# Optimization experiments

Measured on AMD Instinct MI355X. Metric: run time of the kernel, lower is better.

Reference implementation:

```python
import jax, jax.numpy as jnp
import numpy as np

B, IN, H, A, K = 8192, 2048, 256, 8192, 512

def setup_inputs() -> dict:
    key = jax.random.key(0)
    ks = jax.random.split(key, 8)
    s1, s2, s3 = 1.0/np.sqrt(IN), 1.0/np.sqrt(H), 1.0/np.sqrt(H)
    return {
        "x": jax.random.normal(ks[0], (B, IN), dtype=jnp.float32),
        "possible_moves": jax.random.randint(ks[1], (B, K), 0, A, dtype=jnp.int64),
        "W1": jax.random.uniform(ks[2], (IN, H), jnp.float32, -s1, s1),
        "b1": jax.random.uniform(ks[3], (H,), jnp.float32, -s1, s1),
        "W2": jax.random.uniform(ks[4], (H, H), jnp.float32, -s2, s2),
        "b2": jax.random.uniform(ks[5], (H,), jnp.float32, -s2, s2),
        "W3": jax.random.uniform(ks[6], (H, A), jnp.float32, -s3, s3),
        "b3": jax.random.uniform(ks[7], (A,), jnp.float32, -s3, s3),
    }

def reference(x, possible_moves, W1, b1, W2, b2, W3, b3):
    h = jax.nn.relu(x @ W1 + b1)
    h = jax.nn.relu(h @ W2 + b2)
    q = h @ W3 + b3                      # [B, A]
    # build per-sample legal-move mask via scatter (replaces torch python loop)
    rows = jnp.arange(q.shape[0])[:, None]
    mask = jnp.zeros(q.shape, q.dtype).at[rows, possible_moves].set(1.0)
    filtered = q * mask
    # faithful to torch: any exact-zero entry (illegal OR q==0) becomes -inf
    return jnp.where(filtered == 0, -jnp.inf, filtered)
```

## Files before the change

### kernel.cpp

```cpp
#include <hip/hip_runtime.h>
#include <math.h>
#include <stdint.h>

#define B_DIM   8192
#define IN_DIM  2048
#define H_DIM   256
#define A_DIM   8192
#define K_MOVES 512

#define NEG_SENTINEL (-3.0e38f)

typedef __attribute__((ext_vector_type(8))) short      short8;
typedef __attribute__((ext_vector_type(8))) unsigned short ushort8;
typedef __attribute__((ext_vector_type(4))) float      f32x4;

#define MFMA_16x16x32_BF16(a, b, c) \
    __builtin_amdgcn_mfma_f32_16x16x32_bf16((a), (b), (c), 0, 0, 0)

__device__ __forceinline__ unsigned short f2bf(float f) {
    union { float f; unsigned int u; } v; v.f = f;
    unsigned int r = v.u + 0x7fffu + ((v.u >> 16) & 1u);
    return (unsigned short)(r >> 16);
}

__global__ void zero_u64_kernel(unsigned long long* __restrict__ p, int n) {
    int i = blockIdx.x * 256 + threadIdx.x;
    if (i < n) p[i] = 0ULL;
}

__global__ void scatter_mask_kernel(const int* __restrict__ pm,
                                    unsigned long long* __restrict__ mask) {
    int i = blockIdx.x * 256 + threadIdx.x;
    int row = i / K_MOVES;
    int mv  = pm[i];
    if (mv < 0) mv = 0;
    if (mv >= A_DIM) mv = A_DIM - 1;
    atomicOr(&mask[(size_t)row * (A_DIM / 64) + (mv >> 6)],
             1ULL << (mv & 63));
}

__global__ void cvt_bf16_kernel(const float* __restrict__ in,
                                unsigned short* __restrict__ out, int n8) {
    int i = blockIdx.x * 256 + threadIdx.x;
    if (i >= n8) return;
    const float4* p = (const float4*)in + (size_t)i * 2;
    float4 a = p[0], b = p[1];
    ushort8 o;
    o[0] = f2bf(a.x); o[1] = f2bf(a.y); o[2] = f2bf(a.z); o[3] = f2bf(a.w);
    o[4] = f2bf(b.x); o[5] = f2bf(b.y); o[6] = f2bf(b.z); o[7] = f2bf(b.w);
    *(ushort8*)(out + (size_t)i * 8) = o;
}

__global__ __launch_bounds__(256)
void transpose_cvt_kernel(const float* __restrict__ in,
                          unsigned short* __restrict__ out, int R, int C) {
    __shared__ unsigned short tile[32][33];
    int x = blockIdx.x * 32 + threadIdx.x;
#pragma unroll
    for (int i = 0; i < 32; i += 8) {
        int y = blockIdx.y * 32 + threadIdx.y + i;
        tile[threadIdx.y + i][threadIdx.x] = f2bf(in[(size_t)y * C + x]);
    }
    __syncthreads();
    int ox = blockIdx.y * 32 + threadIdx.x;
#pragma unroll
    for (int i = 0; i < 32; i += 8) {
        int oy = blockIdx.x * 32 + threadIdx.y + i;
        out[(size_t)oy * R + ox] = tile[threadIdx.x][threadIdx.y + i];
    }
}

template <int RELU, int MASKED, typename OutT>
__global__ __launch_bounds__(256)
void gemm_bt_mfma(const unsigned short* __restrict__ A,
                  const unsigned short* __restrict__ Bt,
                  const float* __restrict__ bias,
                  OutT* __restrict__ C,
                  const unsigned long long* __restrict__ mask,
                  int M, int N, int K) {
    __shared__ __align__(16) unsigned short As[128 * 32];
    __shared__ __align__(16) unsigned short Bs[128 * 32];

    const int tid  = threadIdx.x;
    const int wave = tid >> 6;
    const int lane = tid & 63;
    const int quad = lane >> 4;
    const int tl   = lane & 15;
    const int wm   = wave >> 1;
    const int wn   = wave & 1;
    const int row0 = blockIdx.y * 128;
    const int col0 = blockIdx.x * 128;

    f32x4 acc[4][4];
#pragma unroll
    for (int i = 0; i < 4; ++i)
#pragma unroll
        for (int j = 0; j < 4; ++j) acc[i][j] = {0.f, 0.f, 0.f, 0.f};

    const int c0 = tid;
    const int c1 = 256 + tid;

    for (int k0 = 0; k0 < K; k0 += 32) {
        {
            const unsigned short* g0 = A + (size_t)(row0 + (c0 >> 2)) * K + k0 + (c0 & 3) * 8;
            const unsigned short* g1 = A + (size_t)(row0 + (c1 >> 2)) * K + k0 + (c1 & 3) * 8;
            __builtin_amdgcn_global_load_lds(
                (const __attribute__((address_space(1))) void*)g0,
                (__attribute__((address_space(3))) void*)&As[(wave * 64) * 8], 16, 0, 0);
            __builtin_amdgcn_global_load_lds(
                (const __attribute__((address_space(1))) void*)g1,
                (__attribute__((address_space(3))) void*)&As[(256 + wave * 64) * 8], 16, 0, 0);
        }
        {
            const unsigned short* g0 = Bt + (size_t)(col0 + (c0 >> 2)) * K + k0 + (c0 & 3) * 8;
            const unsigned short* g1 = Bt + (size_t)(col0 + (c1 >> 2)) * K + k0 + (c1 & 3) * 8;
            __builtin_amdgcn_global_load_lds(
                (const __attribute__((address_space(1))) void*)g0,
                (__attribute__((address_space(3))) void*)&Bs[(wave * 64) * 8], 16, 0, 0);
            __builtin_amdgcn_global_load_lds(
                (const __attribute__((address_space(1))) void*)g1,
                (__attribute__((address_space(3))) void*)&Bs[(256 + wave * 64) * 8], 16, 0, 0);
        }
        __syncthreads();

        short8 af[4], bf[4];
#pragma unroll
        for (int i = 0; i < 4; ++i)
            af[i] = *(const short8*)&As[(wm * 64 + i * 16 + tl) * 32 + quad * 8];
#pragma unroll
        for (int j = 0; j < 4; ++j)
            bf[j] = *(const short8*)&Bs[(wn * 64 + j * 16 + tl) * 32 + quad * 8];

#pragma unroll
        for (int i = 0; i < 4; ++i)
#pragma unroll
            for (int j = 0; j < 4; ++j)
                acc[i][j] = MFMA_16x16x32_BF16(af[i], bf[j], acc[i][j]);
        __syncthreads();
    }

    float bj[4];
#pragma unroll
    for (int j = 0; j < 4; ++j) bj[j] = bias[col0 + wn * 64 + j * 16 + tl];

#pragma unroll
    for (int i = 0; i < 4; ++i) {
#pragma unroll
        for (int reg = 0; reg < 4; ++reg) {
            const int r = row0 + wm * 64 + i * 16 + quad * 4 + reg;
            unsigned long long w = 0;
            if (MASKED) {
                w = mask[(size_t)r * (N >> 6) + (col0 >> 6) + wn];
            }
#pragma unroll
            for (int j = 0; j < 4; ++j) {
                const int c = col0 + wn * 64 + j * 16 + tl;
                float q = acc[i][j][reg] + bj[j];
                if (RELU) q = fmaxf(q, 0.f);
                if (MASKED) {
                    bool legal = (w >> (j * 16 + tl)) & 1ULL;
                    bool ok = legal && (q != 0.f) && (fabsf(q) < 1.0e30f);
                    q = ok ? q : NEG_SENTINEL;
                }
                if constexpr (sizeof(OutT) == 2)
                    C[(size_t)r * N + c] = (OutT)f2bf(q);
                else
                    C[(size_t)r * N + c] = q;
            }
        }
    }
}

extern "C" void kernel_launch(void* const* d_in, const int* in_sizes, int n_in,
                              void* d_out, int out_size, void* d_ws, size_t ws_size,
                              hipStream_t stream) {
    const float* x  = (const float*)d_in[0];
    const int*   pm = (const int*)d_in[1];
    const float* W1 = (const float*)d_in[2];
    const float* b1 = (const float*)d_in[3];
    const float* W2 = (const float*)d_in[4];
    const float* b2 = (const float*)d_in[5];
    const float* W3 = (const float*)d_in[6];
    const float* b3 = (const float*)d_in[7];
    float* out = (float*)d_out;

    char* ws = (char*)d_ws;
    unsigned long long* mask = (unsigned long long*)ws;
    unsigned short* xb  = (unsigned short*)(ws + (8ull  << 20));
    unsigned short* W1t = (unsigned short*)(ws + (40ull << 20));
    unsigned short* W2t = (unsigned short*)(ws + (41ull << 20));
    unsigned short* W3t = (unsigned short*)(ws + (42ull << 20));
    unsigned short* h1b = (unsigned short*)(ws + (46ull << 20));
    unsigned short* h2b = (unsigned short*)(ws + (50ull << 20));

    zero_u64_kernel<<<(B_DIM * (A_DIM / 64)) / 256, 256, 0, stream>>>(
        mask, B_DIM * (A_DIM / 64));
    scatter_mask_kernel<<<(B_DIM * K_MOVES) / 256, 256, 0, stream>>>(pm, mask);

    cvt_bf16_kernel<<<(B_DIM * IN_DIM / 8) / 256, 256, 0, stream>>>(
        x, xb, B_DIM * IN_DIM / 8);
    transpose_cvt_kernel<<<dim3(H_DIM / 32, IN_DIM / 32), dim3(32, 8), 0, stream>>>(
        W1, W1t, IN_DIM, H_DIM);
    transpose_cvt_kernel<<<dim3(H_DIM / 32, H_DIM / 32), dim3(32, 8), 0, stream>>>(
        W2, W2t, H_DIM, H_DIM);
    transpose_cvt_kernel<<<dim3(A_DIM / 32, H_DIM / 32), dim3(32, 8), 0, stream>>>(
        W3, W3t, H_DIM, A_DIM);

    gemm_bt_mfma<1, 0, unsigned short>
        <<<dim3(H_DIM / 128, B_DIM / 128), 256, 0, stream>>>(
        xb, W1t, b1, h1b, nullptr, B_DIM, H_DIM, IN_DIM);

    gemm_bt_mfma<1, 0, unsigned short>
        <<<dim3(H_DIM / 128, B_DIM / 128), 256, 0, stream>>>(
        h1b, W2t, b2, h2b, nullptr, B_DIM, H_DIM, H_DIM);

    gemm_bt_mfma<0, 1, float>
        <<<dim3(A_DIM / 128, B_DIM / 128), 256, 0, stream>>>(
        h2b, W3t, b3, out, mask, B_DIM, A_DIM, H_DIM);
}
```

Baseline: 531.6 us.

## Swap MFMA operands for vectorized row-contiguous epilogue stores and halve M-tile for small GEMMs

Swaps the A/B operands of the MFMA so each lane's four accumulator registers hold four consecutive output columns, which lets the epilogue write float4 or 4-wide bf16 vectors instead of scalar stores. Bias becomes a float4 load, and each lane loads one mask word per row. The row-tile size is also made a template parameter, and the two narrow hidden-layer GEMMs use BM=64 so they launch twice as many blocks. The intent is to cut the cost of the large fp32 output write and to raise occupancy for the small GEMMs, at the price of less reuse per block in those GEMMs.

```diff
diff --git a/kernel.cpp b/kernel.cpp
--- a/kernel.cpp
+++ b/kernel.cpp
@@ -10,9 +10,10 @@
 
 #define NEG_SENTINEL (-3.0e38f)
 
-typedef __attribute__((ext_vector_type(8))) short      short8;
+typedef __attribute__((ext_vector_type(8))) short          short8;
 typedef __attribute__((ext_vector_type(8))) unsigned short ushort8;
-typedef __attribute__((ext_vector_type(4))) float      f32x4;
+typedef __attribute__((ext_vector_type(4))) unsigned short ushort4v;
+typedef __attribute__((ext_vector_type(4))) float          f32x4;
 
 #define MFMA_16x16x32_BF16(a, b, c) \
     __builtin_amdgcn_mfma_f32_16x16x32_bf16((a), (b), (c), 0, 0, 0)
@@ -70,7 +71,7 @@
     }
 }
 
-template <int RELU, int MASKED, typename OutT>
+template <int BM, int RELU, int MASKED, typename OutT>
 __global__ __launch_bounds__(256)
 void gemm_bt_mfma(const unsigned short* __restrict__ A,
                   const unsigned short* __restrict__ Bt,
@@ -78,7 +79,8 @@
                   OutT* __restrict__ C,
                   const unsigned long long* __restrict__ mask,
                   int M, int N, int K) {
-    __shared__ __align__(16) unsigned short As[128 * 32];
+    constexpr int MI = BM / 32;
+    __shared__ __align__(16) unsigned short As[BM * 32];
     __shared__ __align__(16) unsigned short Bs[128 * 32];
 
     const int tid  = threadIdx.x;
@@ -88,84 +90,90 @@
     const int tl   = lane & 15;
     const int wm   = wave >> 1;
     const int wn   = wave & 1;
-    const int row0 = blockIdx.y * 128;
+    const int row0 = blockIdx.y * BM;
     const int col0 = blockIdx.x * 128;
 
-    f32x4 acc[4][4];
-#pragma unroll
-    for (int i = 0; i < 4; ++i)
+    f32x4 acc[MI][4];
+#pragma unroll
+    for (int i = 0; i < MI; ++i)
 #pragma unroll
         for (int j = 0; j < 4; ++j) acc[i][j] = {0.f, 0.f, 0.f, 0.f};
 
-    const int c0 = tid;
-    const int c1 = 256 + tid;
-
     for (int k0 = 0; k0 < K; k0 += 32) {
-        {
-            const unsigned short* g0 = A + (size_t)(row0 + (c0 >> 2)) * K + k0 + (c0 & 3) * 8;
-            const unsigned short* g1 = A + (size_t)(row0 + (c1 >> 2)) * K + k0 + (c1 & 3) * 8;
+#pragma unroll
+        for (int p = 0; p < BM / 64; ++p) {
+            const int c = p * 256 + tid;
+            const unsigned short* g =
+                A + (size_t)(row0 + (c >> 2)) * K + k0 + (c & 3) * 8;
             __builtin_amdgcn_global_load_lds(
-                (const __attribute__((address_space(1))) void*)g0,
-                (__attribute__((address_space(3))) void*)&As[(wave * 64) * 8], 16, 0, 0);
+                (const __attribute__((address_space(1))) void*)g,
+                (__attribute__((address_space(3))) void*)&As[(p * 256 + wave * 64) * 8],
+                16, 0, 0);
+        }
+#pragma unroll
+        for (int p = 0; p < 2; ++p) {
+            const int c = p * 256 + tid;
+            const unsigned short* g =
+                Bt + (size_t)(col0 + (c >> 2)) * K + k0 + (c & 3) * 8;
             __builtin_amdgcn_global_load_lds(
-                (const __attribute__((address_space(1))) void*)g1,
-                (__attribute__((address_space(3))) void*)&As[(256 + wave * 64) * 8], 16, 0, 0);
-        }
-        {
-            const unsigned short* g0 = Bt + (size_t)(col0 + (c0 >> 2)) * K + k0 + (c0 & 3) * 8;
-            const unsigned short* g1 = Bt + (size_t)(col0 + (c1 >> 2)) * K + k0 + (c1 & 3) * 8;
-            __builtin_amdgcn_global_load_lds(
-                (const __attribute__((address_space(1))) void*)g0,
-                (__attribute__((address_space(3))) void*)&Bs[(wave * 64) * 8], 16, 0, 0);
-            __builtin_amdgcn_global_load_lds(
-                (const __attribute__((address_space(1))) void*)g1,
-                (__attribute__((address_space(3))) void*)&Bs[(256 + wave * 64) * 8], 16, 0, 0);
+                (const __attribute__((address_space(1))) void*)g,
+                (__attribute__((address_space(3))) void*)&Bs[(p * 256 + wave * 64) * 8],
+                16, 0, 0);
         }
         __syncthreads();
 
-        short8 af[4], bf[4];
-#pragma unroll
-        for (int i = 0; i < 4; ++i)
-            af[i] = *(const short8*)&As[(wm * 64 + i * 16 + tl) * 32 + quad * 8];
+        short8 af[MI], bf[4];
+#pragma unroll
+        for (int i = 0; i < MI; ++i)
+            af[i] = *(const short8*)&As[(wm * (BM / 2) + i * 16 + tl) * 32 + quad * 8];
 #pragma unroll
         for (int j = 0; j < 4; ++j)
             bf[j] = *(const short8*)&Bs[(wn * 64 + j * 16 + tl) * 32 + quad * 8];
 
 #pragma unroll
-        for (int i = 0; i < 4; ++i)
+        for (int i = 0; i < MI; ++i)
 #pragma unroll
             for (int j = 0; j < 4; ++j)
-                acc[i][j] = MFMA_16x16x32_BF16(af[i], bf[j], acc[i][j]);
+                acc[i][j] = MFMA_16x16x32_BF16(bf[j], af[i], acc[i][j]);
         __syncthreads();
     }
 
-    float bj[4];
-#pragma unroll
-    for (int j = 0; j < 4; ++j) bj[j] = bias[col0 + wn * 64 + j * 16 + tl];
-
-#pragma unroll
-    for (int i = 0; i < 4; ++i) {
-#pragma unroll
-        for (int reg = 0; reg < 4; ++reg) {
-            const int r = row0 + wm * 64 + i * 16 + quad * 4 + reg;
-            unsigned long long w = 0;
-            if (MASKED) {
-                w = mask[(size_t)r * (N >> 6) + (col0 >> 6) + wn];
+    float4 bj4[4];
+#pragma unroll
+    for (int j = 0; j < 4; ++j)
+        bj4[j] = *(const float4*)&bias[col0 + wn * 64 + j * 16 + quad * 4];
+
+#pragma unroll
+    for (int i = 0; i < MI; ++i) {
+        const int r = row0 + wm * (BM / 2) + i * 16 + tl;
+        unsigned long long w = 0;
+        if (MASKED) {
+            w = mask[(size_t)r * (N >> 6) + (col0 >> 6) + wn];
+        }
+#pragma unroll
+        for (int j = 0; j < 4; ++j) {
+            float q[4];
+#pragma unroll
+            for (int reg = 0; reg < 4; ++reg) {
+                float t = acc[i][j][reg] + ((const float*)&bj4[j])[reg];
+                if (RELU) t = fmaxf(t, 0.f);
+                if (MASKED) {
+                    const int bit = j * 16 + quad * 4 + reg;
+                    bool legal = (w >> bit) & 1ULL;
+                    bool ok = legal && (t != 0.f) && (fabsf(t) < 1.0e30f);
+                    t = ok ? t : NEG_SENTINEL;
+                }
+                q[reg] = t;
             }
-#pragma unroll
-            for (int j = 0; j < 4; ++j) {
-                const int c = col0 + wn * 64 + j * 16 + tl;
-                float q = acc[i][j][reg] + bj[j];
-                if (RELU) q = fmaxf(q, 0.f);
-                if (MASKED) {
-                    bool legal = (w >> (j * 16 + tl)) & 1ULL;
-                    bool ok = legal && (q != 0.f) && (fabsf(q) < 1.0e30f);
-                    q = ok ? q : NEG_SENTINEL;
-                }
-                if constexpr (sizeof(OutT) == 2)
-                    C[(size_t)r * N + c] = (OutT)f2bf(q);
-                else
-                    C[(size_t)r * N + c] = q;
+            const size_t off = (size_t)r * N + col0 + wn * 64 + j * 16 + quad * 4;
+            if constexpr (sizeof(OutT) == 2) {
+                ushort4v o;
+                o[0] = f2bf(q[0]); o[1] = f2bf(q[1]);
+                o[2] = f2bf(q[2]); o[3] = f2bf(q[3]);
+                *(ushort4v*)&C[off] = o;
+            } else {
+                float4 o = make_float4(q[0], q[1], q[2], q[3]);
+                *(float4*)&C[off] = o;
             }
         }
     }
@@ -206,15 +214,15 @@
     transpose_cvt_kernel<<<dim3(A_DIM / 32, H_DIM / 32), dim3(32, 8), 0, stream>>>(
         W3, W3t, H_DIM, A_DIM);
 
-    gemm_bt_mfma<1, 0, unsigned short>
-        <<<dim3(H_DIM / 128, B_DIM / 128), 256, 0, stream>>>(
+    gemm_bt_mfma<64, 1, 0, unsigned short>
+        <<<dim3(H_DIM / 128, B_DIM / 64), 256, 0, stream>>>(
         xb, W1t, b1, h1b, nullptr, B_DIM, H_DIM, IN_DIM);
 
-    gemm_bt_mfma<1, 0, unsigned short>
-        <<<dim3(H_DIM / 128, B_DIM / 128), 256, 0, stream>>>(
+    gemm_bt_mfma<64, 1, 0, unsigned short>
+        <<<dim3(H_DIM / 128, B_DIM / 64), 256, 0, stream>>>(
         h1b, W2t, b2, h2b, nullptr, B_DIM, H_DIM, H_DIM);
 
-    gemm_bt_mfma<0, 1, float>
+    gemm_bt_mfma<128, 0, 1, float>
         <<<dim3(A_DIM / 128, B_DIM / 128), 256, 0, stream>>>(
         h2b, W3t, b3, out, mask, B_DIM, A_DIM, H_DIM);
 }
```

New measurement: 517.0 us. 2.7% less time.
